# Performance work log

Measured on AMD Instinct MI355X. Metric: run time of the kernel, lower is better.

## Reference

```python
import jax, jax.numpy as jnp
import numpy as np

N_NODES = 10000
N_EDGES = 80000
IN_DIM, HID, OUT_DIM, HEADS = 768, 512, 768, 4
NEG_SLOPE = 0.2


def setup_inputs() -> dict:
    key = jax.random.key(0)
    ks = jax.random.split(key, 10)
    g = 0.05
    return {
        "x": jax.random.normal(ks[0], (N_NODES, IN_DIM), jnp.float32),
        "edge_index": jax.random.randint(ks[1], (2, N_EDGES), 0, N_NODES, jnp.int64),
        # layer 1: GATConv(768 -> 512, heads=4, concat=True)
        "W1": jax.random.normal(ks[2], (IN_DIM, HEADS * HID), jnp.float32) * g,
        "a1_src": jax.random.normal(ks[3], (HEADS, HID), jnp.float32) * g,
        "a1_dst": jax.random.normal(ks[4], (HEADS, HID), jnp.float32) * g,
        "b1": jnp.zeros((HEADS * HID,), jnp.float32),
        # layer 2: GATConv(2048 -> 768, heads=1, concat=False)
        "W2": jax.random.normal(ks[5], (HEADS * HID, OUT_DIM), jnp.float32) * g,
        "a2_src": jax.random.normal(ks[6], (1, OUT_DIM), jnp.float32) * g,
        "a2_dst": jax.random.normal(ks[7], (1, OUT_DIM), jnp.float32) * g,
        "b2": jnp.zeros((OUT_DIM,), jnp.float32),
    }


def _gat_layer(x, src, dst, W, a_src, a_dst, b, heads, d_out, concat):
    N = x.shape[0]
    h = (x @ W).reshape(N, heads, d_out)              # [N, H, D]
    as_n = jnp.einsum('nhd,hd->nh', h, a_src)          # [N, H]
    ad_n = jnp.einsum('nhd,hd->nh', h, a_dst)
    e = jax.nn.leaky_relu(as_n[src] + ad_n[dst], NEG_SLOPE)  # [E, H]
    # segment softmax over destination nodes
    e_max = jax.lax.stop_gradient(jax.ops.segment_max(e, dst, num_segments=N))
    ex = jnp.exp(e - e_max[dst])
    denom = jax.ops.segment_sum(ex, dst, num_segments=N)
    alpha = ex / (denom[dst] + 1e-16)                  # [E, H]
    msg = alpha[:, :, None] * h[src]                   # [E, H, D]
    out = jax.ops.segment_sum(msg, dst, num_segments=N)  # [N, H, D]
    out = out.reshape(N, heads * d_out) if concat else out.mean(axis=1)
    return out + b


def reference(x, edge_index, W1, a1_src, a1_dst, b1, W2, a2_src, a2_dst, b2):
    N = x.shape[0]
    # PyG GATConv default: add self-loops
    loops = jnp.arange(N, dtype=edge_index.dtype)
    src = jnp.concatenate([edge_index[0], loops])
    dst = jnp.concatenate([edge_index[1], loops])
    h = _gat_layer(x, src, dst, W1, a1_src, a1_dst, b1, HEADS, HID, True)
    h = jax.nn.elu(h)
    out = _gat_layer(h, src, dst, W2, a2_src, a2_dst, b2, 1, OUT_DIM, False)
    return out
```

## Files before the change

### kernel.cpp

```cpp
#include <hip/hip_runtime.h>
#include <hip/hip_bf16.h>

#define N_NODES 10000
#define E_REAL  80000
#define E_TOTAL 90000
#define IN_DIM  768
#define HID     512
#define HEADS   4
#define OUT_DIM 768
#define HD1     (HEADS * HID)
#define NEG_SLOPE 0.2f
#define H1_HSTRIDE (N_NODES * HID)

typedef unsigned short ushort_t;
typedef unsigned int uint_t;

__device__ inline float b2f(ushort_t u) { return __uint_as_float(((uint_t)u) << 16); }
__device__ inline ushort_t f2b(float f) {
    __hip_bfloat16 h = __float2bfloat16(f);
    return *reinterpret_cast<ushort_t*>(&h);
}

__device__ inline void edge_sd(const int* __restrict__ ei, int e, int& s, int& d) {
    if (e < E_REAL) { s = ei[e]; d = ei[E_REAL + e]; }
    else            { s = e - E_REAL; d = s; }
}

#define GLDS(g, l) __builtin_amdgcn_global_load_lds( \
    (const __attribute__((address_space(1))) void*)(g), \
    (__attribute__((address_space(3))) void*)(l), 16, 0, 0)

static const long B_H1B  = 0L;
static const long B_HB   = 40960000L;
static const long B_XB   = 81920000L;
static const long B_W1T  = 97280000L;
static const long B_W2T  = 100425728L;
static const long B_SM   = 103571456L;
static const long SM_AS1   = 0;
static const long SM_AD1   = 40000;
static const long SM_AS2   = 80000;
static const long SM_AD2   = 90000;
static const long SM_CNT   = 100000;
static const long SM_ROWS  = 110000;
static const long SM_CURS  = 120016;
static const long SM_END   = 130016;
static const long B_CSRS = B_SM + SM_END * 4;

__global__ __launch_bounds__(256)
void cast_bf16(const float* __restrict__ in, ushort_t* __restrict__ o, long n) {
    long i = ((long)blockIdx.x * 256 + threadIdx.x) * 8;
    if (i >= n) return;
    float4 v0 = *(const float4*)(in + i);
    float4 v1 = *(const float4*)(in + i + 4);
    ushort_t r[8] = {f2b(v0.x), f2b(v0.y), f2b(v0.z), f2b(v0.w),
                     f2b(v1.x), f2b(v1.y), f2b(v1.z), f2b(v1.w)};
    *(uint4*)(o + i) = *(uint4*)r;
}

__global__ __launch_bounds__(256)
void cast_transpose(const float* __restrict__ W, ushort_t* __restrict__ WT,
                    int K, int N) {
    __shared__ ushort_t t[32][33];
    const int n0 = blockIdx.x * 32, k0 = blockIdx.y * 32;
    const int tx = threadIdx.x & 31, ty = threadIdx.x >> 5;
#pragma unroll
    for (int i = 0; i < 4; ++i) {
        int k = ty + i * 8;
        t[k][tx] = f2b(W[(long)(k0 + k) * N + n0 + tx]);
    }
    __syncthreads();
#pragma unroll
    for (int i = 0; i < 4; ++i) {
        int n = ty + i * 8;
        WT[(long)(n0 + n) * K + k0 + tx] = t[tx][n];
    }
}

typedef short bf16x8 __attribute__((ext_vector_type(8)));
typedef float f32x4 __attribute__((ext_vector_type(4)));

#define BM 128
#define BN 128
#define BK 32

template<int CMODE>
__global__ __launch_bounds__(256)
void gemm_bf16(const ushort_t* __restrict__ A, const ushort_t* __restrict__ BT,
               ushort_t* __restrict__ C, int M, int N, int K) {
    __shared__ ushort_t As[BM * BK];
    __shared__ ushort_t Bs[BN * BK];
    const int tid  = threadIdx.x;
    const int wave = tid >> 6, lane = tid & 63;
    const int quad = lane >> 4, l16 = lane & 15;
    const int bm = blockIdx.y * BM, bn = blockIdx.x * BN;
    const int wr = (wave >> 1) * 64, wc = (wave & 1) * 64;

    const int ch0 = wave * 128 + lane;
    const int ch1 = ch0 + 64;
    const int r0 = ch0 >> 2, c0 = (ch0 & 3) ^ ((r0 >> 1) & 3);
    const int r1 = ch1 >> 2, c1 = (ch1 & 3) ^ ((r1 >> 1) & 3);
    const ushort_t* a0 = A + (long)(bm + r0) * K + c0 * 8;
    const ushort_t* a1 = A + (long)(bm + r1) * K + c1 * 8;
    const ushort_t* b0 = BT + (long)(bn + r0) * K + c0 * 8;
    const ushort_t* b1 = BT + (long)(bn + r1) * K + c1 * 8;
    ushort_t* lA0 = As + (wave * 128) * 8;
    ushort_t* lA1 = As + (wave * 128 + 64) * 8;
    ushort_t* lB0 = Bs + (wave * 128) * 8;
    ushort_t* lB1 = Bs + (wave * 128 + 64) * 8;

    const int swz = (l16 >> 1) & 3;
    f32x4 acc[4][4] = {};

    for (int k0 = 0; k0 < K; k0 += BK) {
        GLDS(a0 + k0, lA0);
        GLDS(a1 + k0, lA1);
        GLDS(b0 + k0, lB0);
        GLDS(b1 + k0, lB1);
        __syncthreads();
        bf16x8 af[4], bfr[4];
#pragma unroll
        for (int i = 0; i < 4; ++i) {
            af[i]  = *(const bf16x8*)(As + ((wr + i * 16 + l16) * 4 + (quad ^ swz)) * 8);
            bfr[i] = *(const bf16x8*)(Bs + ((wc + i * 16 + l16) * 4 + (quad ^ swz)) * 8);
        }
#pragma unroll
        for (int i = 0; i < 4; ++i)
#pragma unroll
            for (int j = 0; j < 4; ++j)
                acc[i][j] = __builtin_amdgcn_mfma_f32_16x16x32_bf16(
                    af[i], bfr[j], acc[i][j], 0, 0, 0);
        __syncthreads();
    }

#pragma unroll
    for (int i = 0; i < 4; ++i) {
#pragma unroll
        for (int r = 0; r < 4; ++r) {
            int row = bm + wr + i * 16 + quad * 4 + r;
            if (row >= M) continue;
#pragma unroll
            for (int j = 0; j < 4; ++j) {
                int col = bn + wc + j * 16 + l16;
                if (CMODE == 0) {
                    C[(long)row * N + col] = f2b(acc[i][j][r]);
                } else {
                    C[(long)(col >> 9) * H1_HSTRIDE + (long)row * HID + (col & 511)]
                        = f2b(acc[i][j][r]);
                }
            }
        }
    }
}

__global__ __launch_bounds__(256)
void attn1(const ushort_t* __restrict__ h, const float* __restrict__ a_s,
           const float* __restrict__ a_d, float* __restrict__ os,
           float* __restrict__ od) {
    const int n = blockIdx.x;
    const int w = threadIdx.x >> 6, lane = threadIdx.x & 63;
    uint4 hv = *(const uint4*)(h + (long)w * H1_HSTRIDE + (long)n * HID + lane * 8);
    const float* asp = a_s + w * HID + lane * 8;
    const float* adp = a_d + w * HID + lane * 8;
    const ushort_t* pb = (const ushort_t*)&hv;
    float ps = 0.f, pd = 0.f;
#pragma unroll
    for (int c = 0; c < 8; ++c) {
        float v = b2f(pb[c]);
        ps += v * asp[c];
        pd += v * adp[c];
    }
#pragma unroll
    for (int off = 32; off > 0; off >>= 1) {
        ps += __shfl_down(ps, off);
        pd += __shfl_down(pd, off);
    }
    if (lane == 0) { os[n * HEADS + w] = ps; od[n * HEADS + w] = pd; }
}

__global__ __launch_bounds__(256)
void attn2(const ushort_t* __restrict__ h, const float* __restrict__ a_s,
           const float* __restrict__ a_d, float* __restrict__ os,
           float* __restrict__ od) {
    __shared__ float rs[4], rd[4];
    const int n = blockIdx.x, tid = threadIdx.x;
    const int w = tid >> 6, lane = tid & 63;
    float ps = 0.f, pd = 0.f;
#pragma unroll
    for (int j = 0; j < 3; ++j) {
        int c = tid + j * 256;
        float v = b2f(h[(long)n * OUT_DIM + c]);
        ps += v * a_s[c];
        pd += v * a_d[c];
    }
#pragma unroll
    for (int off = 32; off > 0; off >>= 1) {
        ps += __shfl_down(ps, off);
        pd += __shfl_down(pd, off);
    }
    if (lane == 0) { rs[w] = ps; rd[w] = pd; }
    __syncthreads();
    if (tid == 0) {
        os[n] = rs[0] + rs[1] + rs[2] + rs[3];
        od[n] = rd[0] + rd[1] + rd[2] + rd[3];
    }
}

__global__ __launch_bounds__(256)
void hist_dst(const int* __restrict__ ei, int* __restrict__ cnt) {
    int e = blockIdx.x * 256 + threadIdx.x;
    if (e >= E_TOTAL) return;
    int s, d; edge_sd(ei, e, s, d);
    atomicAdd(&cnt[d], 1);
}

#define SCAN_CH 40
__global__ __launch_bounds__(256)
void scan_nodes(const int* __restrict__ cnt, int* __restrict__ rows,
                int* __restrict__ curs) {
    __shared__ int part[256];
    const int tid = threadIdx.x;
    const int base = tid * SCAN_CH;
    int local[SCAN_CH];
    int sum = 0;
#pragma unroll
    for (int i = 0; i < SCAN_CH; ++i) {
        int idx = base + i;
        int v = (idx < N_NODES) ? cnt[idx] : 0;
        local[i] = v; sum += v;
    }
    part[tid] = sum;
    __syncthreads();
    for (int off = 1; off < 256; off <<= 1) {
        int v = (tid >= off) ? part[tid - off] : 0;
        __syncthreads();
        part[tid] += v;
        __syncthreads();
    }
    int run = part[tid] - sum;
#pragma unroll
    for (int i = 0; i < SCAN_CH; ++i) {
        int idx = base + i;
        if (idx < N_NODES) { rows[idx] = run; curs[idx] = run; run += local[i]; }
    }
    if (tid == 255) rows[N_NODES] = run;
}

__global__ __launch_bounds__(256)
void scatter_edges(const int* __restrict__ ei, int* __restrict__ curs,
                   int* __restrict__ csr_src) {
    int e = blockIdx.x * 256 + threadIdx.x;
    if (e >= E_TOTAL) return;
    int s, d; edge_sd(ei, e, s, d);
    int pos = atomicAdd(&curs[d], 1);
    csr_src[pos] = s;
}

__global__ __launch_bounds__(64)
void agg1(const int* __restrict__ rows, const int* __restrict__ csr_src,
          const float* __restrict__ as_n, const float* __restrict__ ad_n,
          const ushort_t* __restrict__ hf, const float* __restrict__ b1,
          ushort_t* __restrict__ o) {
    const int n = blockIdx.x, hh = blockIdx.y, lane = threadIdx.x;
    const int beg = rows[n], end = rows[n + 1];
    const ushort_t* hsl = hf + (long)hh * H1_HSTRIDE;
    const float adv = ad_n[(long)n * HEADS + hh];
    float acc[8] = {};
    float dsum = 0.f;
    for (int k = beg; k < end; k += 4) {
        int nk = end - k; if (nk > 4) nk = 4;
        uint4 v[4]; float ex[4];
#pragma unroll
        for (int u = 0; u < 4; ++u) {
            if (u < nk) {
                int s = csr_src[k + u];
                float sc = as_n[(long)s * HEADS + hh] + adv;
                sc = sc > 0.f ? sc : NEG_SLOPE * sc;
                ex[u] = __expf(sc);
                v[u]  = *(const uint4*)(hsl + (long)s * HID + lane * 8);
            }
        }
#pragma unroll
        for (int u = 0; u < 4; ++u) {
            if (u < nk) {
                dsum += ex[u];
                const ushort_t* p = (const ushort_t*)&v[u];
#pragma unroll
                for (int c = 0; c < 8; ++c) acc[c] += ex[u] * b2f(p[c]);
            }
        }
    }
    const float dinv = 1.f / (dsum + 1e-16f);
    const float* bp = b1 + hh * HID + lane * 8;
    ushort_t r[8];
#pragma unroll
    for (int c = 0; c < 8; ++c) {
        float vv = acc[c] * dinv + bp[c];
        r[c] = f2b(vv > 0.f ? vv : expm1f(vv));
    }
    *(uint4*)(o + (long)n * HD1 + hh * HID + lane * 8) = *(uint4*)r;
}

__global__ __launch_bounds__(64)
void agg2(const int* __restrict__ rows, const int* __restrict__ csr_src,
          const float* __restrict__ as_n, const float* __restrict__ ad_n,
          const ushort_t* __restrict__ hf, const float* __restrict__ b2,
          float* __restrict__ out) {
    const int n = blockIdx.x, lane = threadIdx.x;
    const int beg = rows[n], end = rows[n + 1];
    const float adv = ad_n[n];
    float acc[12] = {};
    float dsum = 0.f;
    for (int k = beg; k < end; k += 4) {
        int nk = end - k; if (nk > 4) nk = 4;
        uint4 v4[4]; uint2 v2[4]; float ex[4];
#pragma unroll
        for (int u = 0; u < 4; ++u) {
            if (u < nk) {
                int s = csr_src[k + u];
                float sc = as_n[s] + adv;
                sc = sc > 0.f ? sc : NEG_SLOPE * sc;
                ex[u] = __expf(sc);
                const ushort_t* hp = hf + (long)s * OUT_DIM;
                v4[u] = *(const uint4*)(hp + lane * 8);
                v2[u] = *(const uint2*)(hp + 512 + lane * 4);
            }
        }
#pragma unroll
        for (int u = 0; u < 4; ++u) {
            if (u < nk) {
                dsum += ex[u];
                const ushort_t* p4 = (const ushort_t*)&v4[u];
                const ushort_t* p2 = (const ushort_t*)&v2[u];
#pragma unroll
                for (int c = 0; c < 8; ++c) acc[c] += ex[u] * b2f(p4[c]);
#pragma unroll
                for (int c = 0; c < 4; ++c) acc[8 + c] += ex[u] * b2f(p2[c]);
            }
        }
    }
    const float dinv = 1.f / (dsum + 1e-16f);
    float* op = out + (long)n * OUT_DIM;
#pragma unroll
    for (int c = 0; c < 8; ++c)
        op[lane * 8 + c] = acc[c] * dinv + b2[lane * 8 + c];
#pragma unroll
    for (int c = 0; c < 4; ++c)
        op[512 + lane * 4 + c] = acc[8 + c] * dinv + b2[512 + lane * 4 + c];
}

extern "C" void kernel_launch(void* const* d_in, const int* in_sizes, int n_in,
                              void* d_out, int out_size, void* d_ws, size_t ws_size,
                              hipStream_t stream) {
    const float* x   = (const float*)d_in[0];
    const int*   ei  = (const int*)d_in[1];
    const float* W1  = (const float*)d_in[2];
    const float* a1s = (const float*)d_in[3];
    const float* a1d = (const float*)d_in[4];
    const float* b1  = (const float*)d_in[5];
    const float* W2  = (const float*)d_in[6];
    const float* a2s = (const float*)d_in[7];
    const float* a2d = (const float*)d_in[8];
    const float* b2  = (const float*)d_in[9];
    float* out = (float*)d_out;
    char* base = (char*)d_ws;

    ushort_t* h1b = (ushort_t*)(base + B_H1B);
    ushort_t* hb  = (ushort_t*)(base + B_HB);
    ushort_t* xb  = (ushort_t*)(base + B_XB);
    ushort_t* h2b = xb;
    ushort_t* w1t = (ushort_t*)(base + B_W1T);
    ushort_t* w2t = (ushort_t*)(base + B_W2T);
    float*    sm  = (float*)(base + B_SM);

    float* as1  = sm + SM_AS1;
    float* ad1  = sm + SM_AD1;
    float* as2  = sm + SM_AS2;
    float* ad2  = sm + SM_AD2;
    int* cnt    = (int*)(sm + SM_CNT);
    int* rows   = (int*)(sm + SM_ROWS);
    int* curs   = (int*)(sm + SM_CURS);
    int* csr_src = (int*)(base + B_CSRS);

    hipMemsetAsync(cnt, 0, 10000 * sizeof(int), stream);

    {
        long nx = (long)N_NODES * IN_DIM;
        cast_bf16<<<(int)(nx / 8 / 256 + 1), 256, 0, stream>>>(x, xb, nx);
        cast_transpose<<<dim3(HD1 / 32, IN_DIM / 32), 256, 0, stream>>>(W1, w1t, IN_DIM, HD1);
        cast_transpose<<<dim3(OUT_DIM / 32, HD1 / 32), 256, 0, stream>>>(W2, w2t, HD1, OUT_DIM);
        hist_dst<<<(E_TOTAL + 255) / 256, 256, 0, stream>>>(ei, cnt);
        scan_nodes<<<1, 256, 0, stream>>>(cnt, rows, curs);
        scatter_edges<<<(E_TOTAL + 255) / 256, 256, 0, stream>>>(ei, curs, csr_src);
    }

    gemm_bf16<1><<<dim3(HD1 / BN, (N_NODES + BM - 1) / BM), 256, 0, stream>>>(
        xb, w1t, h1b, N_NODES, HD1, IN_DIM);
    attn1<<<N_NODES, 256, 0, stream>>>(h1b, a1s, a1d, as1, ad1);
    agg1<<<dim3(N_NODES, HEADS), 64, 0, stream>>>(
        rows, csr_src, as1, ad1, h1b, b1, hb);

    gemm_bf16<0><<<dim3(OUT_DIM / BN, (N_NODES + BM - 1) / BM), 256, 0, stream>>>(
        hb, w2t, h2b, N_NODES, OUT_DIM, HD1);
    attn2<<<N_NODES, 256, 0, stream>>>(h2b, a2s, a2d, as2, ad2);
    agg2<<<N_NODES, 64, 0, stream>>>(
        rows, csr_src, as2, ad2, h2b, b2, out);
}
```

Baseline: 343.8 us.

## Fuse attention-score dot products into GEMM epilogue and merge prep kernels

Folds the per-node attention projections (attn1/attn2) into the GEMM epilogue, reducing each row partial across lanes and accumulating it into the score arrays with atomics. This removes a separate pass that reread the bf16 hidden features. The x cast, the two weight transposes and the destination histogram are merged into one prep kernel to cut launch count. The GEMM also switches to a 1D grid that walks groups of 8 row stripes for better L2 reuse of A and B tiles. The cost is extra float atomics per row and head, plus a summation order that is no longer deterministic.

Result: slower. 371.1 us (+8.0%).

```diff
diff --git a/kernel.cpp b/kernel.cpp
--- a/kernel.cpp
+++ b/kernel.cpp
@@ -46,22 +46,16 @@
 static const long SM_END   = 130016;
 static const long B_CSRS = B_SM + SM_END * 4;
 
-__global__ __launch_bounds__(256)
-void cast_bf16(const float* __restrict__ in, ushort_t* __restrict__ o, long n) {
-    long i = ((long)blockIdx.x * 256 + threadIdx.x) * 8;
-    if (i >= n) return;
-    float4 v0 = *(const float4*)(in + i);
-    float4 v1 = *(const float4*)(in + i + 4);
-    ushort_t r[8] = {f2b(v0.x), f2b(v0.y), f2b(v0.z), f2b(v0.w),
-                     f2b(v1.x), f2b(v1.y), f2b(v1.z), f2b(v1.w)};
-    *(uint4*)(o + i) = *(uint4*)r;
-}
-
-__global__ __launch_bounds__(256)
-void cast_transpose(const float* __restrict__ W, ushort_t* __restrict__ WT,
-                    int K, int N) {
+#define PREP_CAST   3750
+#define PREP_T1     (PREP_CAST + 1536)
+#define PREP_T2     (PREP_T1 + 1536)
+#define PREP_BLOCKS (PREP_T2 + 352)
+
+__device__ inline void do_transpose(const float* __restrict__ W,
+                                    ushort_t* __restrict__ WT,
+                                    int K, int N, int bx, int by) {
     __shared__ ushort_t t[32][33];
-    const int n0 = blockIdx.x * 32, k0 = blockIdx.y * 32;
+    const int n0 = bx * 32, k0 = by * 32;
     const int tx = threadIdx.x & 31, ty = threadIdx.x >> 5;
 #pragma unroll
     for (int i = 0; i < 4; ++i) {
@@ -76,6 +70,34 @@
     }
 }
 
+__global__ __launch_bounds__(256)
+void prep(const float* __restrict__ x, ushort_t* __restrict__ xb,
+          const float* __restrict__ W1, ushort_t* __restrict__ w1t,
+          const float* __restrict__ W2, ushort_t* __restrict__ w2t,
+          const int* __restrict__ ei, int* __restrict__ cnt) {
+    const int bid = blockIdx.x;
+    if (bid < PREP_CAST) {
+        long i = ((long)bid * 256 + threadIdx.x) * 8;
+        float4 v0 = *(const float4*)(x + i);
+        float4 v1 = *(const float4*)(x + i + 4);
+        ushort_t r[8] = {f2b(v0.x), f2b(v0.y), f2b(v0.z), f2b(v0.w),
+                         f2b(v1.x), f2b(v1.y), f2b(v1.z), f2b(v1.w)};
+        *(uint4*)(xb + i) = *(uint4*)r;
+    } else if (bid < PREP_T1) {
+        int b = bid - PREP_CAST;
+        do_transpose(W1, w1t, IN_DIM, HD1, b & 63, b >> 6);
+    } else if (bid < PREP_T2) {
+        int b = bid - PREP_T1;
+        do_transpose(W2, w2t, HD1, OUT_DIM, b % 24, b / 24);
+    } else {
+        int e = (bid - PREP_T2) * 256 + threadIdx.x;
+        if (e < E_TOTAL) {
+            int s, d; edge_sd(ei, e, s, d);
+            atomicAdd(&cnt[d], 1);
+        }
+    }
+}
+
 typedef short bf16x8 __attribute__((ext_vector_type(8)));
 typedef float f32x4 __attribute__((ext_vector_type(4)));
 
@@ -86,13 +108,21 @@
 template<int CMODE>
 __global__ __launch_bounds__(256)
 void gemm_bf16(const ushort_t* __restrict__ A, const ushort_t* __restrict__ BT,
-               ushort_t* __restrict__ C, int M, int N, int K) {
+               ushort_t* __restrict__ C, int M, int N, int K,
+               const float* __restrict__ a_s, const float* __restrict__ a_d,
+               float* __restrict__ os, float* __restrict__ od) {
     __shared__ ushort_t As[BM * BK];
     __shared__ ushort_t Bs[BN * BK];
+    const int CB = N / BN;
+    const int bid = blockIdx.x;
+    const int sg = bid / (8 * CB), wi = bid % (8 * CB);
+    const int stripe = sg * 8 + (wi & 7);
+    const int bm = stripe * BM, bn = (wi >> 3) * BN;
+    if (bm >= M) return;
+
     const int tid  = threadIdx.x;
     const int wave = tid >> 6, lane = tid & 63;
     const int quad = lane >> 4, l16 = lane & 15;
-    const int bm = blockIdx.y * BM, bn = blockIdx.x * BN;
     const int wr = (wave >> 1) * 64, wc = (wave & 1) * 64;
 
     const int ch0 = wave * 128 + lane;
@@ -150,67 +180,47 @@
             }
         }
     }
-}
-
-__global__ __launch_bounds__(256)
-void attn1(const ushort_t* __restrict__ h, const float* __restrict__ a_s,
-           const float* __restrict__ a_d, float* __restrict__ os,
-           float* __restrict__ od) {
-    const int n = blockIdx.x;
-    const int w = threadIdx.x >> 6, lane = threadIdx.x & 63;
-    uint4 hv = *(const uint4*)(h + (long)w * H1_HSTRIDE + (long)n * HID + lane * 8);
-    const float* asp = a_s + w * HID + lane * 8;
-    const float* adp = a_d + w * HID + lane * 8;
-    const ushort_t* pb = (const ushort_t*)&hv;
-    float ps = 0.f, pd = 0.f;
-#pragma unroll
-    for (int c = 0; c < 8; ++c) {
-        float v = b2f(pb[c]);
-        ps += v * asp[c];
-        pd += v * adp[c];
-    }
-#pragma unroll
-    for (int off = 32; off > 0; off >>= 1) {
-        ps += __shfl_down(ps, off);
-        pd += __shfl_down(pd, off);
-    }
-    if (lane == 0) { os[n * HEADS + w] = ps; od[n * HEADS + w] = pd; }
-}
-
-__global__ __launch_bounds__(256)
-void attn2(const ushort_t* __restrict__ h, const float* __restrict__ a_s,
-           const float* __restrict__ a_d, float* __restrict__ os,
-           float* __restrict__ od) {
-    __shared__ float rs[4], rd[4];
-    const int n = blockIdx.x, tid = threadIdx.x;
-    const int w = tid >> 6, lane = tid & 63;
-    float ps = 0.f, pd = 0.f;
-#pragma unroll
-    for (int j = 0; j < 3; ++j) {
-        int c = tid + j * 256;
-        float v = b2f(h[(long)n * OUT_DIM + c]);
-        ps += v * a_s[c];
-        pd += v * a_d[c];
-    }
-#pragma unroll
-    for (int off = 32; off > 0; off >>= 1) {
-        ps += __shfl_down(ps, off);
-        pd += __shfl_down(pd, off);
-    }
-    if (lane == 0) { rs[w] = ps; rd[w] = pd; }
-    __syncthreads();
-    if (tid == 0) {
-        os[n] = rs[0] + rs[1] + rs[2] + rs[3];
-        od[n] = rd[0] + rd[1] + rd[2] + rd[3];
-    }
-}
-
-__global__ __launch_bounds__(256)
-void hist_dst(const int* __restrict__ ei, int* __restrict__ cnt) {
-    int e = blockIdx.x * 256 + threadIdx.x;
-    if (e >= E_TOTAL) return;
-    int s, d; edge_sd(ei, e, s, d);
-    atomicAdd(&cnt[d], 1);
+
+    const int cbase = bn + wc;
+    const int hidx = (CMODE == 1) ? (cbase >> 9) : 0;
+    const float* aS = (CMODE == 1) ? a_s + hidx * HID : a_s;
+    const float* aD = (CMODE == 1) ? a_d + hidx * HID : a_d;
+    float asv[4], adv[4];
+#pragma unroll
+    for (int j = 0; j < 4; ++j) {
+        int col = cbase + j * 16 + l16;
+        int ch = (CMODE == 1) ? (col & 511) : col;
+        asv[j] = aS[ch]; adv[j] = aD[ch];
+    }
+#pragma unroll
+    for (int i = 0; i < 4; ++i) {
+#pragma unroll
+        for (int r = 0; r < 4; ++r) {
+            float ss = 0.f, sd = 0.f;
+#pragma unroll
+            for (int j = 0; j < 4; ++j) {
+                float v = acc[i][j][r];
+                ss += v * asv[j]; sd += v * adv[j];
+            }
+#pragma unroll
+            for (int m = 8; m >= 1; m >>= 1) {
+                ss += __shfl_xor(ss, m);
+                sd += __shfl_xor(sd, m);
+            }
+            if (l16 == 0) {
+                int row = bm + wr + i * 16 + quad * 4 + r;
+                if (row < M) {
+                    if (CMODE == 1) {
+                        atomicAdd(&os[row * HEADS + hidx], ss);
+                        atomicAdd(&od[row * HEADS + hidx], sd);
+                    } else {
+                        atomicAdd(&os[row], ss);
+                        atomicAdd(&od[row], sd);
+                    }
+                }
+            }
+        }
+    }
 }
 
 #define SCAN_CH 40
@@ -381,27 +391,19 @@
     int* curs   = (int*)(sm + SM_CURS);
     int* csr_src = (int*)(base + B_CSRS);
 
-    hipMemsetAsync(cnt, 0, 10000 * sizeof(int), stream);
-
-    {
-        long nx = (long)N_NODES * IN_DIM;
-        cast_bf16<<<(int)(nx / 8 / 256 + 1), 256, 0, stream>>>(x, xb, nx);
-        cast_transpose<<<dim3(HD1 / 32, IN_DIM / 32), 256, 0, stream>>>(W1, w1t, IN_DIM, HD1);
-        cast_transpose<<<dim3(OUT_DIM / 32, HD1 / 32), 256, 0, stream>>>(W2, w2t, HD1, OUT_DIM);
-        hist_dst<<<(E_TOTAL + 255) / 256, 256, 0, stream>>>(ei, cnt);
-        scan_nodes<<<1, 256, 0, stream>>>(cnt, rows, curs);
-        scatter_edges<<<(E_TOTAL + 255) / 256, 256, 0, stream>>>(ei, curs, csr_src);
-    }
-
-    gemm_bf16<1><<<dim3(HD1 / BN, (N_NODES + BM - 1) / BM), 256, 0, stream>>>(
-        xb, w1t, h1b, N_NODES, HD1, IN_DIM);
-    attn1<<<N_NODES, 256, 0, stream>>>(h1b, a1s, a1d, as1, ad1);
+    hipMemsetAsync(sm, 0, 110000 * sizeof(float), stream);
+
+    prep<<<PREP_BLOCKS, 256, 0, stream>>>(x, xb, W1, w1t, W2, w2t, ei, cnt);
+    scan_nodes<<<1, 256, 0, stream>>>(cnt, rows, curs);
+    scatter_edges<<<(E_TOTAL + 255) / 256, 256, 0, stream>>>(ei, curs, csr_src);
+
+    gemm_bf16<1><<<10 * 8 * (HD1 / BN), 256, 0, stream>>>(
+        xb, w1t, h1b, N_NODES, HD1, IN_DIM, a1s, a1d, as1, ad1);
     agg1<<<dim3(N_NODES, HEADS), 64, 0, stream>>>(
         rows, csr_src, as1, ad1, h1b, b1, hb);
 
-    gemm_bf16<0><<<dim3(OUT_DIM / BN, (N_NODES + BM - 1) / BM), 256, 0, stream>>>(
-        hb, w2t, h2b, N_NODES, OUT_DIM, HD1);
-    attn2<<<N_NODES, 256, 0, stream>>>(h2b, a2s, a2d, as2, ad2);
+    gemm_bf16<0><<<10 * 8 * (OUT_DIM / BN), 256, 0, stream>>>(
+        hb, w2t, h2b, N_NODES, OUT_DIM, HD1, a2s, a2d, as2, ad2);
     agg2<<<N_NODES, 64, 0, stream>>>(
         rows, csr_src, as2, ad2, h2b, b2, out);
 }
```
